# Kernel tuning notes

Measured on AMD Instinct MI355X. Metric: run time of the kernel, lower is better.

## Reference

```python
import jax, jax.numpy as jnp
import numpy as np

SCALE = 30.0
MARGIN = 0.5
COS_M = float(np.cos(MARGIN))
SIN_M = float(np.sin(MARGIN))
TH = float(np.cos(np.pi - MARGIN))
MM = float(np.sin(np.pi - MARGIN) * MARGIN)
LN_EPS = 1e-7

B, S, H = 16, 2048, 1024
N_SPANS = 64
N_CLASSES = 4096


def setup_inputs() -> dict:
    key = jax.random.key(0)
    k1, k2, k3, k4, k5 = jax.random.split(key, 5)
    encoder_layer = jax.random.normal(k1, (B, S, H), dtype=jnp.float32)
    ln_gamma = jnp.ones((H,), jnp.float32)
    ln_beta = jnp.zeros((H,), jnp.float32)
    # xavier-uniform-like init for arcface head weight [out, in]
    limit = float(np.sqrt(6.0 / (N_CLASSES + H)))
    arc_weight = jax.random.uniform(k2, (N_CLASSES, H), jnp.float32, -limit, limit)
    heads = jax.random.randint(k3, (B, N_SPANS), 0, S - 32).astype(jnp.int32)
    lens = jax.random.randint(k4, (B, N_SPANS), 1, 33).astype(jnp.int32)
    tails = heads + lens  # guaranteed head < tail <= S
    labels = jax.random.randint(k5, (B, N_SPANS), 0, N_CLASSES).astype(jnp.int32)
    return {
        "encoder_layer": encoder_layer,
        "ln_gamma": ln_gamma,
        "ln_beta": ln_beta,
        "arc_weight": arc_weight,
        "span_head_idxs": heads,
        "span_tail_idxs": tails,
        "labels": labels,
    }


def _span_mean(encoder_layer, heads, tails):
    # fused ragged segment-mean via inclusive prefix sums over the seq dim
    # csum: [B, S+1, H], csum[b, t] = sum of encoder_layer[b, :t]
    csum = jnp.concatenate(
        [jnp.zeros_like(encoder_layer[:, :1]), jnp.cumsum(encoder_layer, axis=1)], axis=1
    )
    gather = lambda idx: jnp.take_along_axis(csum, idx[:, :, None].astype(jnp.int32), axis=1)
    sums = gather(tails) - gather(heads)  # [B, n_spans, H]
    counts = (tails - heads).astype(encoder_layer.dtype)[:, :, None]
    return sums / counts


def _layer_norm(x, gamma, beta):
    mu = jnp.mean(x, axis=-1, keepdims=True)
    var = jnp.mean(jnp.square(x - mu), axis=-1, keepdims=True)
    return (x - mu) * jax.lax.rsqrt(var + LN_EPS) * gamma + beta


def _l2norm(x):
    return x / jnp.maximum(jnp.linalg.norm(x, axis=-1, keepdims=True), 1e-12)


def reference(encoder_layer, ln_gamma, ln_beta, arc_weight, span_head_idxs, span_tail_idxs, labels):
    emb = _span_mean(encoder_layer, span_head_idxs, span_tail_idxs)  # [B, n_spans, H]
    emb = _layer_norm(emb, ln_gamma, ln_beta)
    emb = emb.reshape(-1, emb.shape[-1])  # [B*n_spans, H]
    lab = labels.reshape(-1)
    # ArcMarginProduct: cosine similarity
    cosine = (_l2norm(emb) @ _l2norm(arc_weight).T).astype(jnp.float32)  # [N, C]
    sine = jnp.sqrt(jnp.clip(1.0 - jnp.square(cosine), 0.0))
    phi = cosine * COS_M - sine * SIN_M
    phi = jnp.where(cosine > TH, phi, cosine - MM)
    onehot = jax.nn.one_hot(lab, cosine.shape[-1], dtype=cosine.dtype)
    logits = (onehot * phi + (1.0 - onehot) * cosine) * SCALE
    # mean cross entropy (all labels valid, ignore_index unused)
    logp = jax.nn.log_softmax(logits, axis=-1)
    nll = -jnp.take_along_axis(logp, lab[:, None].astype(jnp.int32), axis=1)[:, 0]
    return jnp.mean(nll)
```

## Files before the change

### kernel.cpp

```cpp
#include <hip/hip_runtime.h>
#include <hip/hip_bf16.h>
#include <math.h>

#define B_     16
#define S_     2048
#define H_     1024
#define NS_    64
#define NC_    4096
#define NROWS  1024

#define SCALE_ 30.0f
#define COS_M_ 0.8775825618903728f
#define SIN_M_ 0.479425538604203f
#define TH_    (-0.8775825618903728f)
#define MM_    0.2397127693021015f
#define LN_EPS_ 1e-7f


__device__ __forceinline__ unsigned short f2bf(float f) {
    union { float f; unsigned int u; } v; v.f = f;
    unsigned int r = v.u + 0x7fffu + ((v.u >> 16) & 1u);
    return (unsigned short)(r >> 16);
}

__device__ __forceinline__ float block_sum(float v) {
    __shared__ float sb[4];
    #pragma unroll
    for (int off = 32; off > 0; off >>= 1) v += __shfl_down(v, off, 64);
    if ((threadIdx.x & 63) == 0) sb[threadIdx.x >> 6] = v;
    __syncthreads();
    float r = sb[0] + sb[1] + sb[2] + sb[3];
    __syncthreads();
    return r;
}

__device__ __forceinline__ float block_max(float v) {
    __shared__ float sb[4];
    #pragma unroll
    for (int off = 32; off > 0; off >>= 1) v = fmaxf(v, __shfl_down(v, off, 64));
    if ((threadIdx.x & 63) == 0) sb[threadIdx.x >> 6] = v;
    __syncthreads();
    float r = fmaxf(fmaxf(sb[0], sb[1]), fmaxf(sb[2], sb[3]));
    __syncthreads();
    return r;
}

__device__ __forceinline__ void gload16(const void* g, void* l) {
    __builtin_amdgcn_global_load_lds(
        (const __attribute__((address_space(1))) unsigned int*)g,
        (__attribute__((address_space(3))) unsigned int*)l,
        16, 0, 0);
}

typedef short bf16x8 __attribute__((ext_vector_type(8)));
typedef float f32x4  __attribute__((ext_vector_type(4)));

__global__ __launch_bounds__(256) void span_kernel(
    const float* __restrict__ enc,
    const float* __restrict__ gamma,
    const float* __restrict__ beta,
    const int*   __restrict__ heads,
    const int*   __restrict__ tails,
    unsigned short* __restrict__ embn)
{
    const int span = blockIdx.x;
    const int b    = span >> 6;
    const int head = heads[span];
    const int tail = tails[span];
    const int cnt  = tail - head;
    const int tid  = threadIdx.x;

    const float4* base = (const float4*)(enc + ((size_t)b * S_ + head) * H_);
    float4 a; a.x = 0.f; a.y = 0.f; a.z = 0.f; a.w = 0.f;
    for (int s = 0; s < cnt; ++s) {
        float4 x = base[s * (H_ / 4) + tid];
        a.x += x.x; a.y += x.y; a.z += x.z; a.w += x.w;
    }
    const float inv = 1.0f / (float)cnt;
    float v0 = a.x * inv, v1 = a.y * inv, v2 = a.z * inv, v3 = a.w * inv;

    float mu = block_sum(v0 + v1 + v2 + v3) * (1.0f / H_);
    float d0 = v0 - mu, d1 = v1 - mu, d2 = v2 - mu, d3 = v3 - mu;
    float var = block_sum(d0*d0 + d1*d1 + d2*d2 + d3*d3) * (1.0f / H_);
    float rstd = rsqrtf(var + LN_EPS_);

    const int h = tid * 4;
    float y0 = d0 * rstd * gamma[h+0] + beta[h+0];
    float y1 = d1 * rstd * gamma[h+1] + beta[h+1];
    float y2 = d2 * rstd * gamma[h+2] + beta[h+2];
    float y3 = d3 * rstd * gamma[h+3] + beta[h+3];

    float ss = block_sum(y0*y0 + y1*y1 + y2*y2 + y3*y3);
    float invn = 1.0f / fmaxf(sqrtf(ss), 1e-12f);

    ushort4 o;
    o.x = f2bf(y0 * invn); o.y = f2bf(y1 * invn);
    o.z = f2bf(y2 * invn); o.w = f2bf(y3 * invn);
    *(ushort4*)(embn + (size_t)span * H_ + h) = o;
}

__global__ __launch_bounds__(256) void wnorm_kernel(
    const float* __restrict__ W,
    unsigned short* __restrict__ Wn)
{
    const int row = blockIdx.x;
    const int tid = threadIdx.x;
    float4 x = ((const float4*)(W + (size_t)row * H_))[tid];
    float ss = block_sum(x.x*x.x + x.y*x.y + x.z*x.z + x.w*x.w);
    float invn = 1.0f / fmaxf(sqrtf(ss), 1e-12f);
    ushort4 o;
    o.x = f2bf(x.x * invn); o.y = f2bf(x.y * invn);
    o.z = f2bf(x.z * invn); o.w = f2bf(x.w * invn);
    *(ushort4*)(Wn + (size_t)row * H_ + tid * 4) = o;
}

__global__ __launch_bounds__(256, 1) void gemm_kernel(
    const unsigned short* __restrict__ A,
    const unsigned short* __restrict__ Bw,
    float* __restrict__ C)
{
    __shared__ short As[128 * 32];
    __shared__ short Bs[128 * 32];

    const int m0   = blockIdx.x * 128;
    const int n0   = blockIdx.y * 128;
    const int tid  = threadIdx.x;
    const int lane = tid & 63;
    const int w    = tid >> 6;
    const int wm   = (w & 1) * 64;
    const int wn   = (w >> 1) * 64;
    const int lrow = lane & 15;
    const int q    = lane >> 4;

    const int rowA   = tid >> 2;
    const int kchunk = (tid & 3) * 8;

    f32x4 acc[4][4];
    #pragma unroll
    for (int i = 0; i < 4; ++i)
        #pragma unroll
        for (int j = 0; j < 4; ++j)
            acc[i][j] = (f32x4){0.f, 0.f, 0.f, 0.f};

    for (int k0 = 0; k0 < 1024; k0 += 32) {
        __syncthreads();
        #pragma unroll
        for (int t = 0; t < 2; ++t) {
            const int r = t * 64 + rowA;
            gload16(A  + ((size_t)(m0 + r) * 1024 + k0 + kchunk), &As[r * 32 + kchunk]);
            gload16(Bw + ((size_t)(n0 + r) * 1024 + k0 + kchunk), &Bs[r * 32 + kchunk]);
        }
        __syncthreads();

        bf16x8 af[4], bfr[4];
        #pragma unroll
        for (int i = 0; i < 4; ++i)
            af[i] = *(const bf16x8*)(&As[(wm + i * 16 + lrow) * 32 + q * 8]);
        #pragma unroll
        for (int j = 0; j < 4; ++j)
            bfr[j] = *(const bf16x8*)(&Bs[(wn + j * 16 + lrow) * 32 + q * 8]);

        #pragma unroll
        for (int i = 0; i < 4; ++i)
            #pragma unroll
            for (int j = 0; j < 4; ++j)
                acc[i][j] = __builtin_amdgcn_mfma_f32_16x16x32_bf16(af[i], bfr[j], acc[i][j], 0, 0, 0);
    }

    #pragma unroll
    for (int i = 0; i < 4; ++i) {
        const int rbase = m0 + wm + i * 16 + q * 4;
        #pragma unroll
        for (int j = 0; j < 4; ++j) {
            const int col = n0 + wn + j * 16 + lrow;
            #pragma unroll
            for (int r2 = 0; r2 < 4; ++r2)
                C[(size_t)(rbase + r2) * NC_ + col] = acc[i][j][r2];
        }
    }
}

__global__ __launch_bounds__(256) void ce_kernel(
    const float* __restrict__ cosine,
    const int*   __restrict__ labels,
    float* __restrict__ nll)
{
    __shared__ float s_lab;
    const int row = blockIdx.x;
    const int lab = labels[row];
    const int tid = threadIdx.x;
    const float4* c4 = (const float4*)(cosine + (size_t)row * NC_);

    float vals[16];
    float m = -1e30f;
    #pragma unroll
    for (int t = 0; t < 4; ++t) {
        float4 x = c4[tid + t * 256];
        const int cbase = (tid + t * 256) * 4;
        float xs[4] = {x.x, x.y, x.z, x.w};
        #pragma unroll
        for (int k = 0; k < 4; ++k) {
            float c = xs[k];
            float logit = c;
            if (cbase + k == lab) {
                float sine = sqrtf(fmaxf(1.0f - c * c, 0.0f));
                float phi  = c * COS_M_ - sine * SIN_M_;
                logit = (c > TH_) ? phi : (c - MM_);
            }
            logit *= SCALE_;
            vals[t * 4 + k] = logit;
            if (cbase + k == lab) s_lab = logit;
            m = fmaxf(m, logit);
        }
    }
    float gm = block_max(m);
    float e = 0.f;
    #pragma unroll
    for (int t = 0; t < 16; ++t) e += expf(vals[t] - gm);
    float se = block_sum(e);
    if (tid == 0) nll[row] = logf(se) + gm - s_lab;
}

__global__ __launch_bounds__(256) void mean_kernel(
    const float* __restrict__ nll, float* __restrict__ out)
{
    const int tid = threadIdx.x;
    float s = 0.f;
    #pragma unroll
    for (int t = 0; t < 4; ++t) s += nll[tid + t * 256];
    float tot = block_sum(s);
    if (tid == 0) out[0] = tot * (1.0f / NROWS);
}

extern "C" void kernel_launch(void* const* d_in, const int* in_sizes, int n_in,
                              void* d_out, int out_size, void* d_ws, size_t ws_size,
                              hipStream_t stream) {
    const float* enc    = (const float*)d_in[0];
    const float* gamma  = (const float*)d_in[1];
    const float* beta   = (const float*)d_in[2];
    const float* W      = (const float*)d_in[3];
    const int*   heads  = (const int*)d_in[4];
    const int*   tails  = (const int*)d_in[5];
    const int*   labels = (const int*)d_in[6];
    float* out = (float*)d_out;

    char* ws = (char*)d_ws;
    unsigned short* embn   = (unsigned short*)(ws);
    unsigned short* Wn     = (unsigned short*)(ws + (2u  << 20));
    float*          cosine = (float*)        (ws + (10u << 20));
    float*          nllbuf = (float*)        (ws + (26u << 20));

    span_kernel <<<NROWS, 256, 0, stream>>>(enc, gamma, beta, heads, tails, embn);
    wnorm_kernel<<<NC_,   256, 0, stream>>>(W, Wn);
    dim3 g3(NROWS / 128, NC_ / 128);
    gemm_kernel <<<g3,    256, 0, stream>>>(embn, Wn, cosine);
    ce_kernel   <<<NROWS, 256, 0, stream>>>(cosine, labels, nllbuf);
    mean_kernel <<<1,     256, 0, stream>>>(nllbuf, out);
}
```

Baseline: 235.1 us.

## Fuse norm kernels and double-buffer GEMM with swizzled LDS and block remap

```diff
diff --git a/kernel.cpp b/kernel.cpp
--- a/kernel.cpp
+++ b/kernel.cpp
@@ -1,5 +1,4 @@
 #include <hip/hip_runtime.h>
-#include <hip/hip_bf16.h>
 #include <math.h>
 
 #define B_     16
@@ -55,63 +54,71 @@
 typedef short bf16x8 __attribute__((ext_vector_type(8)));
 typedef float f32x4  __attribute__((ext_vector_type(4)));
 
-__global__ __launch_bounds__(256) void span_kernel(
+__global__ __launch_bounds__(256) void fused_norm_kernel(
     const float* __restrict__ enc,
     const float* __restrict__ gamma,
     const float* __restrict__ beta,
     const int*   __restrict__ heads,
     const int*   __restrict__ tails,
-    unsigned short* __restrict__ embn)
-{
-    const int span = blockIdx.x;
-    const int b    = span >> 6;
-    const int head = heads[span];
-    const int tail = tails[span];
-    const int cnt  = tail - head;
-    const int tid  = threadIdx.x;
-
-    const float4* base = (const float4*)(enc + ((size_t)b * S_ + head) * H_);
-    float4 a; a.x = 0.f; a.y = 0.f; a.z = 0.f; a.w = 0.f;
-    for (int s = 0; s < cnt; ++s) {
-        float4 x = base[s * (H_ / 4) + tid];
-        a.x += x.x; a.y += x.y; a.z += x.z; a.w += x.w;
-    }
-    const float inv = 1.0f / (float)cnt;
-    float v0 = a.x * inv, v1 = a.y * inv, v2 = a.z * inv, v3 = a.w * inv;
-
-    float mu = block_sum(v0 + v1 + v2 + v3) * (1.0f / H_);
-    float d0 = v0 - mu, d1 = v1 - mu, d2 = v2 - mu, d3 = v3 - mu;
-    float var = block_sum(d0*d0 + d1*d1 + d2*d2 + d3*d3) * (1.0f / H_);
-    float rstd = rsqrtf(var + LN_EPS_);
-
-    const int h = tid * 4;
-    float y0 = d0 * rstd * gamma[h+0] + beta[h+0];
-    float y1 = d1 * rstd * gamma[h+1] + beta[h+1];
-    float y2 = d2 * rstd * gamma[h+2] + beta[h+2];
-    float y3 = d3 * rstd * gamma[h+3] + beta[h+3];
-
-    float ss = block_sum(y0*y0 + y1*y1 + y2*y2 + y3*y3);
-    float invn = 1.0f / fmaxf(sqrtf(ss), 1e-12f);
-
-    ushort4 o;
-    o.x = f2bf(y0 * invn); o.y = f2bf(y1 * invn);
-    o.z = f2bf(y2 * invn); o.w = f2bf(y3 * invn);
-    *(ushort4*)(embn + (size_t)span * H_ + h) = o;
-}
-
-__global__ __launch_bounds__(256) void wnorm_kernel(
     const float* __restrict__ W,
+    unsigned short* __restrict__ embn,
     unsigned short* __restrict__ Wn)
 {
-    const int row = blockIdx.x;
     const int tid = threadIdx.x;
-    float4 x = ((const float4*)(W + (size_t)row * H_))[tid];
-    float ss = block_sum(x.x*x.x + x.y*x.y + x.z*x.z + x.w*x.w);
-    float invn = 1.0f / fmaxf(sqrtf(ss), 1e-12f);
-    ushort4 o;
-    o.x = f2bf(x.x * invn); o.y = f2bf(x.y * invn);
-    o.z = f2bf(x.z * invn); o.w = f2bf(x.w * invn);
-    *(ushort4*)(Wn + (size_t)row * H_ + tid * 4) = o;
+
+    if (blockIdx.x < NROWS) {
+        const int span = blockIdx.x;
+        const int b    = span >> 6;
+        const int head = heads[span];
+        const int tail = tails[span];
+        const int cnt  = tail - head;
+
+        const float4* base = (const float4*)(enc + ((size_t)b * S_ + head) * H_) + tid;
+        float a0x=0.f,a0y=0.f,a0z=0.f,a0w=0.f;
+        float a1x=0.f,a1y=0.f,a1z=0.f,a1w=0.f;
+        int s = 0;
+        for (; s + 2 <= cnt; s += 2) {
+            float4 x = base[(size_t)s       * (H_ / 4)];
+            float4 y = base[(size_t)(s + 1) * (H_ / 4)];
+            a0x += x.x; a0y += x.y; a0z += x.z; a0w += x.w;
+            a1x += y.x; a1y += y.y; a1z += y.z; a1w += y.w;
+        }
+        if (s < cnt) {
+            float4 x = base[(size_t)s * (H_ / 4)];
+            a0x += x.x; a0y += x.y; a0z += x.z; a0w += x.w;
+        }
+        const float inv = 1.0f / (float)cnt;
+        float v0 = (a0x + a1x) * inv, v1 = (a0y + a1y) * inv;
+        float v2 = (a0z + a1z) * inv, v3 = (a0w + a1w) * inv;
+
+        float mu = block_sum(v0 + v1 + v2 + v3) * (1.0f / H_);
+        float d0 = v0 - mu, d1 = v1 - mu, d2 = v2 - mu, d3 = v3 - mu;
+        float var = block_sum(d0*d0 + d1*d1 + d2*d2 + d3*d3) * (1.0f / H_);
+        float rstd = rsqrtf(var + LN_EPS_);
+
+        const int h = tid * 4;
+        float y0 = d0 * rstd * gamma[h+0] + beta[h+0];
+        float y1 = d1 * rstd * gamma[h+1] + beta[h+1];
+        float y2 = d2 * rstd * gamma[h+2] + beta[h+2];
+        float y3 = d3 * rstd * gamma[h+3] + beta[h+3];
+
+        float ss = block_sum(y0*y0 + y1*y1 + y2*y2 + y3*y3);
+        float invn = 1.0f / fmaxf(sqrtf(ss), 1e-12f);
+
+        ushort4 o;
+        o.x = f2bf(y0 * invn); o.y = f2bf(y1 * invn);
+        o.z = f2bf(y2 * invn); o.w = f2bf(y3 * invn);
+        *(ushort4*)(embn + (size_t)span * H_ + h) = o;
+    } else {
+        const int row = blockIdx.x - NROWS;
+        float4 x = ((const float4*)(W + (size_t)row * H_))[tid];
+        float ss = block_sum(x.x*x.x + x.y*x.y + x.z*x.z + x.w*x.w);
+        float invn = 1.0f / fmaxf(sqrtf(ss), 1e-12f);
+        ushort4 o;
+        o.x = f2bf(x.x * invn); o.y = f2bf(x.y * invn);
+        o.z = f2bf(x.z * invn); o.w = f2bf(x.w * invn);
+        *(ushort4*)(Wn + (size_t)row * H_ + tid * 4) = o;
+    }
 }
 
 __global__ __launch_bounds__(256, 1) void gemm_kernel(
@@ -119,11 +126,14 @@
     const unsigned short* __restrict__ Bw,
     float* __restrict__ C)
 {
-    __shared__ short As[128 * 32];
-    __shared__ short Bs[128 * 32];
-
-    const int m0   = blockIdx.x * 128;
-    const int n0   = blockIdx.y * 128;
+    __shared__ short As[2][128 * 64];
+    __shared__ short Bs[2][128 * 64];
+
+    const int bid = blockIdx.y * 8 + blockIdx.x;
+    const int swz = (bid & 7) * 32 + (bid >> 3);
+    const int m0  = (swz & 7) * 128;
+    const int n0  = (swz >> 3) * 128;
+
     const int tid  = threadIdx.x;
     const int lane = tid & 63;
     const int w    = tid >> 6;
@@ -131,9 +141,10 @@
     const int wn   = (w >> 1) * 64;
     const int lrow = lane & 15;
     const int q    = lane >> 4;
-
-    const int rowA   = tid >> 2;
-    const int kchunk = (tid & 3) * 8;
+    const int xr   = lrow & 7;
+
+    const int srow = tid >> 3;
+    const int sc16 = tid & 7;
 
     f32x4 acc[4][4];
     #pragma unroll
@@ -142,30 +153,50 @@
         for (int j = 0; j < 4; ++j)
             acc[i][j] = (f32x4){0.f, 0.f, 0.f, 0.f};
 
-    for (int k0 = 0; k0 < 1024; k0 += 32) {
-        __syncthreads();
-        #pragma unroll
-        for (int t = 0; t < 2; ++t) {
-            const int r = t * 64 + rowA;
-            gload16(A  + ((size_t)(m0 + r) * 1024 + k0 + kchunk), &As[r * 32 + kchunk]);
-            gload16(Bw + ((size_t)(n0 + r) * 1024 + k0 + kchunk), &Bs[r * 32 + kchunk]);
-        }
-        __syncthreads();
-
-        bf16x8 af[4], bfr[4];
-        #pragma unroll
-        for (int i = 0; i < 4; ++i)
-            af[i] = *(const bf16x8*)(&As[(wm + i * 16 + lrow) * 32 + q * 8]);
-        #pragma unroll
-        for (int j = 0; j < 4; ++j)
-            bfr[j] = *(const bf16x8*)(&Bs[(wn + j * 16 + lrow) * 32 + q * 8]);
-
-        #pragma unroll
-        for (int i = 0; i < 4; ++i)
+    auto stage = [&](int bsel, int k0) {
+        #pragma unroll
+        for (int i = 0; i < 4; ++i) {
+            const int row = i * 32 + srow;
+            const int s16 = sc16 ^ (row & 7);
+            gload16(A  + (size_t)(m0 + row) * 1024 + k0 + s16 * 8,
+                    &As[bsel][row * 64 + sc16 * 8]);
+            gload16(Bw + (size_t)(n0 + row) * 1024 + k0 + s16 * 8,
+                    &Bs[bsel][row * 64 + sc16 * 8]);
+        }
+    };
+
+    auto compute = [&](int bsel) {
+        #pragma unroll
+        for (int kk = 0; kk < 2; ++kk) {
+            const int c16 = ((kk << 2) | q) ^ xr;
+            bf16x8 af[4], bfr[4];
+            #pragma unroll
+            for (int i = 0; i < 4; ++i)
+                af[i] = *(const bf16x8*)(&As[bsel][(wm + i * 16 + lrow) * 64 + c16 * 8]);
             #pragma unroll
             for (int j = 0; j < 4; ++j)
-                acc[i][j] = __builtin_amdgcn_mfma_f32_16x16x32_bf16(af[i], bfr[j], acc[i][j], 0, 0, 0);
-    }
+                bfr[j] = *(const bf16x8*)(&Bs[bsel][(wn + j * 16 + lrow) * 64 + c16 * 8]);
+            #pragma unroll
+            for (int i = 0; i < 4; ++i)
+                #pragma unroll
+                for (int j = 0; j < 4; ++j)
+                    acc[i][j] = __builtin_amdgcn_mfma_f32_16x16x32_bf16(af[i], bfr[j], acc[i][j], 0, 0, 0);
+        }
+    };
+
+    stage(0, 0);
+    asm volatile("s_waitcnt vmcnt(0)" ::: "memory");
+    __builtin_amdgcn_s_barrier();
+
+    int cur = 0;
+    for (int t = 0; t < 15; ++t) {
+        stage(cur ^ 1, (t + 1) * 64);
+        compute(cur);
+        asm volatile("s_waitcnt vmcnt(0)" ::: "memory");
+        __builtin_amdgcn_s_barrier();
+        cur ^= 1;
+    }
+    compute(cur);
 
     #pragma unroll
     for (int i = 0; i < 4; ++i) {
@@ -250,10 +281,9 @@
     float*          cosine = (float*)        (ws + (10u << 20));
     float*          nllbuf = (float*)        (ws + (26u << 20));
 
-    span_kernel <<<NROWS, 256, 0, stream>>>(enc, gamma, beta, heads, tails, embn);
-    wnorm_kernel<<<NC_,   256, 0, stream>>>(W, Wn);
-    dim3 g3(NROWS / 128, NC_ / 128);
-    gemm_kernel <<<g3,    256, 0, stream>>>(embn, Wn, cosine);
+    fused_norm_kernel<<<NROWS + NC_, 256, 0, stream>>>(enc, gamma, beta, heads, tails, W, embn, Wn);
+    dim3 g3(8, 32);
+    gemm_kernel <<<g3,  256, 0, stream>>>(embn, Wn, cosine);
     ce_kernel   <<<NROWS, 256, 0, stream>>>(cosine, labels, nllbuf);
     mean_kernel <<<1,     256, 0, stream>>>(nllbuf, out);
 }
```

Result: faster. 227.7 us (-3.2%).
